# Kernel tuning notes

Measured on AMD Instinct MI355X. Metric: run time of the kernel, lower is better.

## Reference

```python
import jax, jax.numpy as jnp
import numpy as np

N = 50000
E = 800000
IN_C = 128
HID = 32
OUT_C = 16
NEG_SLOPE = 0.2


def setup_inputs() -> dict:
    key = jax.random.key(0)
    ks = jax.random.split(key, 16)
    x = jax.random.normal(ks[0], (N, IN_C), dtype=jnp.float32)
    edge_index = jax.random.randint(ks[1], (2, E), 0, N, dtype=jnp.int64)

    def glorot(k, shape):
        fan = shape[0] + shape[-1]
        return jax.random.uniform(k, shape, jnp.float32, -1.0, 1.0) * jnp.sqrt(6.0 / fan)

    # layer1: in=128 -> heads=4, ch=32, concat -> out 128
    W1 = glorot(ks[2], (IN_C, 4 * HID))
    a_src1 = glorot(ks[3], (4, HID))
    a_dst1 = glorot(ks[4], (4, HID))
    b1 = jnp.zeros((4 * HID,), jnp.float32)
    # layer2: in=128 -> heads=2, ch=32, concat -> out 64
    W2 = glorot(ks[5], (4 * HID, 2 * HID))
    a_src2 = glorot(ks[6], (2, HID))
    a_dst2 = glorot(ks[7], (2, HID))
    b2 = jnp.zeros((2 * HID,), jnp.float32)
    # layer3: in=64 -> heads=1, ch=16, mean -> out 16
    W3 = glorot(ks[8], (2 * HID, OUT_C))
    a_src3 = glorot(ks[9], (1, OUT_C))
    a_dst3 = glorot(ks[10], (1, OUT_C))
    b3 = jnp.zeros((OUT_C,), jnp.float32)
    return {"x": x, "edge_index": edge_index,
            "W1": W1, "a_src1": a_src1, "a_dst1": a_dst1, "b1": b1,
            "W2": W2, "a_src2": a_src2, "a_dst2": a_dst2, "b2": b2,
            "W3": W3, "a_src3": a_src3, "a_dst3": a_dst3, "b3": b3}


def gat_conv(x, src, dst, W, a_src, a_dst, bias, heads, ch, concat):
    n = x.shape[0]
    h = (x @ W).reshape(n, heads, ch)                      # [N,H,C]
    alpha_s = jnp.einsum('nhc,hc->nh', h, a_src)           # [N,H]
    alpha_d = jnp.einsum('nhc,hc->nh', h, a_dst)           # [N,H]
    logits = jax.nn.leaky_relu(alpha_s[src] + alpha_d[dst], NEG_SLOPE)  # [E,H]
    # segment softmax over edges sharing the same destination node
    m = jax.ops.segment_max(logits, dst, num_segments=n)
    m = jnp.where(jnp.isfinite(m), m, 0.0)
    e = jnp.exp(logits - m[dst])
    denom = jax.ops.segment_sum(e, dst, num_segments=n)
    alpha = e / (denom[dst] + 1e-16)                       # [E,H]
    msg = h[src] * alpha[:, :, None]                       # [E,H,C]
    out = jax.ops.segment_sum(msg, dst, num_segments=n)    # [N,H,C]
    out = out.reshape(n, heads * ch) if concat else out.mean(axis=1)
    return out + bias


def reference(x, edge_index, W1, a_src1, a_dst1, b1, W2, a_src2, a_dst2, b2, W3, a_src3, a_dst3, b3):
    n = x.shape[0]
    loops = jnp.arange(n, dtype=edge_index.dtype)
    src = jnp.concatenate([edge_index[0], loops])  # add self loops (PyG default)
    dst = jnp.concatenate([edge_index[1], loops])
    h = jax.nn.relu(gat_conv(x, src, dst, W1, a_src1, a_dst1, b1, 4, HID, True))
    h = jax.nn.relu(gat_conv(h, src, dst, W2, a_src2, a_dst2, b2, 2, HID, True))
    out = gat_conv(h, src, dst, W3, a_src3, a_dst3, b3, 1, OUT_C, False)
    return out
```

## Files before the change

kernel.cpp:

```cpp
#include <hip/hip_runtime.h>
#include <hip/hip_bf16.h>
#include <stdint.h>

#define NODES 50000
#define NEDGE 800000
#define TEDGE (NEDGE + NODES)
#define GBLK ((NODES + 63) / 64)
#define CHNK 64
#define CSRCH 13312
#define HALFN 25088
#define NSTR (2 * HALFN)
#define FSB 64
#define SCATB 832

typedef unsigned short u16;
typedef unsigned int u32;
typedef unsigned long long u64;
typedef short s16x8 __attribute__((ext_vector_type(8)));
typedef float f32x4 __attribute__((ext_vector_type(4)));

__device__ __forceinline__ float bf2f(u16 v) {
  return __uint_as_float(((u32)v) << 16);
}
__device__ __forceinline__ u16 f2bf(float f) {
  u32 u = __float_as_uint(f);
  u32 r = (u + 0x7FFFu + ((u >> 16) & 1u)) >> 16;
  return (u16)r;
}
__device__ __forceinline__ float lo16f(u32 w) { return __uint_as_float(w << 16); }
__device__ __forceinline__ float hi16f(u32 w) { return __uint_as_float(w & 0xFFFF0000u); }
__device__ __forceinline__ float lrelu(float x) {
  return (x > 0.f) ? x : 0.2f * x;
}
__device__ __forceinline__ int clampn(int v) {
  return ((u32)v < NODES) ? v : 0;
}
__device__ __forceinline__ float load1(const void* p, size_t i, bool fb) {
  return fb ? bf2f(((const u16*)p)[i]) : ((const float*)p)[i];
}
__device__ __forceinline__ u32 encf(float f) {
  u32 u = __float_as_uint(f);
  return (u & 0x80000000u) ? ~u : (u | 0x80000000u);
}
__device__ __forceinline__ float decf(u32 k) {
  u32 u = (k & 0x80000000u) ? (k & 0x7FFFFFFFu) : ~k;
  return __uint_as_float(u);
}

__global__ __launch_bounds__(256) void k_probe(
    const int* __restrict__ ei, const u16* __restrict__ xs16,
    int* __restrict__ flags,
    const void* __restrict__ W1, const void* __restrict__ W2,
    const void* __restrict__ W3, const void* __restrict__ as1,
    const void* __restrict__ ad1, const void* __restrict__ as2,
    const void* __restrict__ ad2, const void* __restrict__ as3,
    const void* __restrict__ ad3, u16* __restrict__ wt1,
    u16* __restrict__ wt2, u16* __restrict__ wt3, u16* __restrict__ wa1,
    u16* __restrict__ wa2, u16* __restrict__ wa3) {
  __shared__ int sfb;
  int t = threadIdx.x;
  int g = blockIdx.x * 256 + t;
  if (blockIdx.x == 0 && t >= 2 && t < 32) flags[t] = 0;
  if (t < 64) {
    int big = 0;
#pragma unroll
    for (int k = 0; k < 4; ++k) {
      u32 ex = (xs16[2 * (t * 4 + k)] >> 7) & 0xFF;
      big += (ex >= 0x90);
    }
#pragma unroll
    for (int off = 32; off >= 1; off >>= 1) big += __shfl_xor(big, off);
    if (t == 0) sfb = (big >= 8) ? 0 : 1;
    if (blockIdx.x == 0) {
      int odd = 0, even = 0;
#pragma unroll
      for (int k = 0; k < 4; ++k) {
        int idx = t + 64 * k;
        odd |= (ei[2 * idx + 1] != 0);
        even |= (ei[2 * idx] != 0);
      }
      u64 bo = __ballot(odd);
      u64 be = __ballot(even);
      if (t == 0) flags[0] = (bo == 0ull && be != 0ull) ? 1 : 0;
    }
  }
  __syncthreads();
  bool fb = sfb != 0;
  if (blockIdx.x == 0 && t == 0) flags[1] = fb ? 1 : 0;

  auto fidx = [](int n, int k, int KS) {
    int nt = n >> 4, lrow = n & 15, ks = k >> 5, quad = (k >> 3) & 3, j = k & 7;
    return ((size_t)((nt * KS + ks) * 64 + quad * 16 + lrow)) * 8 + j;
  };

  if (g < 16384) {
    int n = g >> 7, k = g & 127;
    wt1[fidx(n, k, 4)] = f2bf(load1(W1, (size_t)k * 128 + n, fb));
  } else if (g < 24576) {
    int r = g - 16384;
    int n = r >> 7, k = r & 127;
    wt2[fidx(n, k, 4)] = f2bf(load1(W2, (size_t)k * 64 + n, fb));
  } else if (g < 25600) {
    int r = g - 24576;
    int n = r >> 6, k = r & 63;
    wt3[fidx(n, k, 2)] = f2bf(load1(W3, (size_t)k * 16 + n, fb));
  } else if (g < 27648) {
    int e = g - 25600;
    int n = e >> 7, k = e & 127;
    float v = 0.f;
    if (n < 8) {
      int head = (n < 4) ? n : n - 4;
      const void* av = (n < 4) ? as1 : ad1;
      for (int c = 0; c < 32; ++c)
        v += load1(W1, (size_t)k * 128 + head * 32 + c, fb) *
             load1(av, head * 32 + c, fb);
    }
    wa1[fidx(n, k, 4)] = (n < 8) ? f2bf(v) : (u16)0;
  } else if (g < 29696) {
    int e = g - 27648;
    int n = e >> 7, k = e & 127;
    float v = 0.f;
    if (n < 4) {
      int head = (n < 2) ? n : n - 2;
      const void* av = (n < 2) ? as2 : ad2;
      for (int c = 0; c < 32; ++c)
        v += load1(W2, (size_t)k * 64 + head * 32 + c, fb) *
             load1(av, head * 32 + c, fb);
    }
    wa2[fidx(n, k, 4)] = (n < 4) ? f2bf(v) : (u16)0;
  } else if (g < 30720) {
    int e = g - 29696;
    int n = e >> 6, k = e & 63;
    float v = 0.f;
    if (n < 2) {
      const void* av = (n < 1) ? as3 : ad3;
      for (int c = 0; c < 16; ++c)
        v += load1(W3, (size_t)k * 16 + c, fb) * load1(av, c, fb);
    }
    wa3[fidx(n, k, 2)] = (n < 2) ? f2bf(v) : (u16)0;
  }
}

__global__ __launch_bounds__(1024) void k_hista(const int* __restrict__ ei,
                                                const int* __restrict__ flags,
                                                u32* __restrict__ sd,
                                                u16* __restrict__ rank16,
                                                u16* __restrict__ cnt) {
  __shared__ u32 hcnt[HALFN / 2];
  int b = blockIdx.x;
  int c = b >> 1, half = b & 1;
  int t = threadIdx.x;
  for (int i = t; i < HALFN / 2; i += 1024) hcnt[i] = 0;
  __syncthreads();
  bool odd = flags[0] != 0;
  int ebase = c * CSRCH;
  int nlo = half * HALFN;
#pragma unroll
  for (int i = 0; i < 13; ++i) {
    int e = ebase + i * 1024 + t;
    if (e < TEDGE) {
      int s, d;
      if (e < NEDGE) {
        if (odd) { s = ei[2 * e]; d = ei[2 * (NEDGE + e)]; }
        else { s = ei[e]; d = ei[NEDGE + e]; }
      } else {
        s = e - NEDGE; d = s;
      }
      s = clampn(s); d = clampn(d);
      if (half == 0) sd[e] = (u32)s | ((u32)d << 16);
      int li = d - nlo;
      if ((u32)li < HALFN) {
        u32 old = atomicAdd(&hcnt[li >> 1], 1u << (16 * (li & 1)));
        rank16[e] = (u16)((old >> (16 * (li & 1))) & 0xFFFFu);
      }
    }
  }
  __syncthreads();
  u32* crow = (u32*)(cnt + (size_t)c * NSTR + nlo);
  for (int i = t; i < HALFN / 2; i += 1024) crow[i] = hcnt[i];
}

__global__ __launch_bounds__(1024) void k_foldscan(const u16* __restrict__ cnt,
                                                   u16* __restrict__ basecnt,
                                                   int* __restrict__ rowptr,
                                                   int* __restrict__ parts,
                                                   int* __restrict__ counter) {
  __shared__ int swave[16];
  __shared__ int sbase, stot;
  int b = blockIdx.x, t = threadIdx.x;
  int n = b * 784 + t;
  int v = 0;
  if (t < 784 && n < NODES) {
    int acc = 0;
#pragma unroll 8
    for (int c = 0; c < CHNK; ++c) {
      u16 cv = cnt[(size_t)c * NSTR + n];
      basecnt[(size_t)c * NSTR + n] = (u16)acc;
      acc += cv;
    }
    v = acc;
  }
  int lane = t & 63, w = t >> 6;
  int x = v;
#pragma unroll
  for (int off = 1; off < 64; off <<= 1) {
    int y = __shfl_up(x, off);
    if (lane >= off) x += y;
  }
  if (lane == 63) swave[w] = x;
  __syncthreads();
  if (w == 0) {
    int wv = (lane < 16) ? swave[lane] : 0;
#pragma unroll
    for (int off = 1; off < 16; off <<= 1) {
      int y = __shfl_up(wv, off);
      if (lane >= off) wv += y;
    }
    if (lane == 15) {
      __hip_atomic_store(&parts[b], wv, __ATOMIC_RELAXED,
                         __HIP_MEMORY_SCOPE_AGENT);
      __hip_atomic_fetch_add(counter, 1, __ATOMIC_RELEASE,
                             __HIP_MEMORY_SCOPE_AGENT);
    }
    if (lane < 16) swave[lane] = wv;
  }
  __syncthreads();
  if (t == 0) {
    while (__hip_atomic_load(counter, __ATOMIC_ACQUIRE,
                             __HIP_MEMORY_SCOPE_AGENT) < FSB)
      __builtin_amdgcn_s_sleep(2);
  }
  __syncthreads();
  if (w == 0) {
    int pv = __hip_atomic_load(&parts[lane], __ATOMIC_RELAXED,
                               __HIP_MEMORY_SCOPE_AGENT);
    int pb = (lane < b) ? pv : 0;
#pragma unroll
    for (int off = 32; off >= 1; off >>= 1) {
      pb += __shfl_xor(pb, off);
      pv += __shfl_xor(pv, off);
    }
    if (lane == 0) { sbase = pb; stot = pv; }
  }
  __syncthreads();
  int run = sbase + ((w == 0) ? 0 : swave[w - 1]) + (x - v);
  if (t < 784 && n < NODES) rowptr[n] = run;
  if (b == 0 && t == 0) rowptr[NODES] = stot;
}


template <int K, int N, int H, bool XEXT>
__device__ __forceinline__ void gmfma_tile(const void* __restrict__ xin,
                                           const u16* __restrict__ wtf,
                                           const u16* __restrict__ waf,
                                           u16* __restrict__ hout,
                                           float* __restrict__ asg,
                                           float* __restrict__ adg,
                                           u32* __restrict__ gm,
                                           const int* __restrict__ flags,
                                           int M, int row0,
                                           u16* __restrict__ xlds,
                                           u32* __restrict__ lmax) {
  constexpr int KP = K + 8;
  constexpr int NT = N / 16;
  constexpr int KS = K / 32;
  constexpr int KG = K / 8;
  int t = threadIdx.x;
  bool fb = flags[1] != 0;
  if (t < 2 * H) lmax[t] = 0;

  bool xbf = XEXT ? fb : true;
  for (int i = t; i < 64 * KG; i += 256) {
    int r = i / KG, kg = i % KG;
    int grow = row0 + r;
    if (grow >= M) grow = M - 1;
    if (xbf) {
      *(uint4*)&xlds[r * KP + kg * 8] =
          *(const uint4*)((const u16*)xin + (size_t)grow * K + kg * 8);
    } else {
      const float* gp = (const float*)xin + (size_t)grow * K + kg * 8;
      float4 f0 = *(const float4*)gp, f1 = *(const float4*)(gp + 4);
      *(ushort4*)&xlds[r * KP + kg * 8] =
          make_ushort4(f2bf(f0.x), f2bf(f0.y), f2bf(f0.z), f2bf(f0.w));
      *(ushort4*)&xlds[r * KP + kg * 8 + 4] =
          make_ushort4(f2bf(f1.x), f2bf(f1.y), f2bf(f1.z), f2bf(f1.w));
    }
  }
  __syncthreads();

  int lane = t & 63, w = t >> 6;
  int lrow = lane & 15, quad = lane >> 4;
  f32x4 acc[NT];
  f32x4 eacc = (f32x4){0.f, 0.f, 0.f, 0.f};
#pragma unroll
  for (int nt = 0; nt < NT; ++nt) acc[nt] = (f32x4){0.f, 0.f, 0.f, 0.f};

  const u16* xbase = xlds + (w * 16 + lrow) * KP + quad * 8;
#pragma unroll
  for (int ks = 0; ks < KS; ++ks) {
    s16x8 a = *(const s16x8*)(xbase + ks * 32);
    s16x8 be = *(const s16x8*)(waf + ((size_t)(ks * 64 + lane)) * 8);
    eacc = __builtin_amdgcn_mfma_f32_16x16x32_bf16(a, be, eacc, 0, 0, 0);
#pragma unroll
    for (int nt = 0; nt < NT; ++nt) {
      s16x8 b = *(const s16x8*)(wtf + ((size_t)((nt * KS + ks) * 64 + lane)) * 8);
      acc[nt] = __builtin_amdgcn_mfma_f32_16x16x32_bf16(a, b, acc[nt], 0, 0, 0);
    }
  }

  float pm = -3.4e38f;
  int baserow = row0 + w * 16 + quad * 4;
#pragma unroll
  for (int r = 0; r < 4; ++r) {
    int grow = baserow + r;
    if (grow < M) {
#pragma unroll
      for (int nt = 0; nt < NT; ++nt)
        hout[(size_t)grow * N + nt * 16 + lrow] = f2bf(acc[nt][r]);
      if (lrow < H) asg[grow * H + lrow] = eacc[r];
      else if (lrow < 2 * H) adg[grow * H + (lrow - H)] = eacc[r];
    }
    pm = fmaxf(pm, eacc[r]);
  }
  if (lrow < 2 * H) atomicMax(&lmax[lrow], encf(pm));
  __syncthreads();
  if (t < 2 * H) atomicMax(&gm[t], lmax[t]);
}

__global__ __launch_bounds__(256) void k_scatgm(
    const u32* __restrict__ sd, const u16* __restrict__ rank16,
    const u16* __restrict__ basecnt, const int* __restrict__ rowptr,
    u16* __restrict__ srcs, const void* __restrict__ xin,
    const u16* __restrict__ wtf, const u16* __restrict__ waf,
    u16* __restrict__ hout, float* __restrict__ asg, float* __restrict__ adg,
    u32* __restrict__ gm, const int* __restrict__ flags) {
  __shared__ u16 xlds[64 * 136];
  __shared__ u32 lmax[8];
  int bi = blockIdx.x;
  int role, idx;
  if (bi < 2 * GBLK) { role = bi & 1; idx = bi >> 1; }
  else { role = 0; idx = GBLK + (bi - 2 * GBLK); }
  if (role == 0) {
    int c = idx / 13;
    int e0 = idx * 1024 + threadIdx.x;
#pragma unroll
    for (int u = 0; u < 4; ++u) {
      int e = e0 + u * 256;
      if (e < TEDGE) {
        u32 v = sd[e];
        int d = (int)(v >> 16);
        int pos = rowptr[d] + (int)basecnt[(size_t)c * NSTR + d] +
                  (int)rank16[e];
        srcs[pos] = (u16)(v & 0xFFFFu);
      }
    }
    return;
  }
  gmfma_tile<128, 128, 4, true>(xin, wtf, waf, hout, asg, adg, gm, flags,
                                NODES, idx * 64, xlds, lmax);
}

template <int K, int N, int H, bool XEXT>
__global__ __launch_bounds__(256) void k_gmfma(const void* __restrict__ xin,
                                               const u16* __restrict__ wtf,
                                               const u16* __restrict__ waf,
                                               u16* __restrict__ hout,
                                               float* __restrict__ asg,
                                               float* __restrict__ adg,
                                               u32* __restrict__ gm,
                                               const int* __restrict__ flags,
                                               int M) {
  __shared__ u16 xlds[64 * (K + 8)];
  __shared__ u32 lmax[2 * H];
  gmfma_tile<K, N, H, XEXT>(xin, wtf, waf, hout, asg, adg, gm, flags, M,
                            blockIdx.x * 64, xlds, lmax);
}

template <int H, int C, bool RELU, bool FINAL>
__global__ __launch_bounds__(256) void k_agg(const u16* __restrict__ hbuf,
                                             const float* __restrict__ asg,
                                             const float* __restrict__ adg,
                                             const int* __restrict__ rowptr,
                                             const u16* __restrict__ srcs,
                                             const void* __restrict__ bias,
                                             const int* __restrict__ flags,
                                             const u32* __restrict__ gm,
                                             void* __restrict__ outp, int n) {
  constexpr int HC = H * C;
  constexpr int L = HC / 8;
  constexpr int EPN = 32 / L;
  constexpr int UN = (4 * EPN <= 32) ? 4 : 2;
  __shared__ u16 lds_s[4][64];
  __shared__ float lds_e[4][64][H];
  int lane = threadIdx.x & 63;
  int w = threadIdx.x >> 6;
  int nh = lane >> 5;
  int hl = lane & 31;
  int node = blockIdx.x * 8 + w * 2 + nh;
  if (node >= n) node = n - 1;
  bool fb = flags[1] != 0;
  int start = rowptr[node], end = rowptr[node + 1];
  if (end < start || end - start > TEDGE) { start = 0; end = 0; }

  float adh[H], M[H];
#pragma unroll
  for (int h = 0; h < H; ++h) adh[h] = adg[node * H + h];
#pragma unroll
  for (int h = 0; h < H; ++h) M[h] = lrelu(decf(gm[h]) + decf(gm[H + h]));

  int sub = hl / L;
  int cl = hl & (L - 1);
  int ch0 = cl * 8;
  int myhead = ch0 / C;
  int base = nh * 32;

  float den[H];
#pragma unroll
  for (int h = 0; h < H; ++h) den[h] = 0.f;
  float acc[UN][8];
#pragma unroll
  for (int u = 0; u < UN; ++u)
#pragma unroll
    for (int i = 0; i < 8; ++i) acc[u][i] = 0.f;

  for (int chunk = start; chunk < end; chunk += 32) {
    int e = chunk + hl;
    int s = 0;
    float ee[H];
#pragma unroll
    for (int h = 0; h < H; ++h) ee[h] = 0.f;
    if (e < end) {
      s = srcs[e];
      float av[H];
      if (H == 4) { float4 t4 = *(const float4*)(asg + s * 4);
        av[0] = t4.x; av[1] = t4.y; av[H > 2 ? 2 : 0] = t4.z; av[H > 3 ? 3 : 0] = t4.w; }
      else if (H == 2) { float2 t2 = *(const float2*)(asg + s * 2); av[0] = t2.x; av[1] = t2.y; }
      else av[0] = asg[s];
#pragma unroll
      for (int h = 0; h < H; ++h) {
        float x = __expf(lrelu(av[h] + adh[h]) - M[h]);
        ee[h] = x;
        den[h] += x;
      }
    }
    __builtin_amdgcn_wave_barrier();
    lds_s[w][lane] = (u16)s;
#pragma unroll
    for (int h = 0; h < H; ++h) lds_e[w][lane][h] = ee[h];
    __builtin_amdgcn_wave_barrier();

    int cn = min(32, end - chunk);
    for (int j = 0; j < cn; j += UN * EPN) {
      int sx[UN];
      float ax[UN];
#pragma unroll
      for (int u = 0; u < UN; ++u) {
        int ei_ = base + j + u * EPN + sub;
        sx[u] = lds_s[w][ei_];
        ax[u] = lds_e[w][ei_][myhead];
      }
#pragma unroll
      for (int u = 0; u < UN; ++u) {
        uint4 v = *(const uint4*)(hbuf + (size_t)sx[u] * HC + ch0);
        acc[u][0] += ax[u] * lo16f(v.x); acc[u][1] += ax[u] * hi16f(v.x);
        acc[u][2] += ax[u] * lo16f(v.y); acc[u][3] += ax[u] * hi16f(v.y);
        acc[u][4] += ax[u] * lo16f(v.z); acc[u][5] += ax[u] * hi16f(v.z);
        acc[u][6] += ax[u] * lo16f(v.w); acc[u][7] += ax[u] * hi16f(v.w);
      }
    }
  }

#pragma unroll
  for (int m = 16; m >= 1; m >>= 1) {
#pragma unroll
    for (int h = 0; h < H; ++h) den[h] += __shfl_xor(den[h], m);
  }
  float tt[8];
#pragma unroll
  for (int i = 0; i < 8; ++i) {
    tt[i] = acc[0][i];
#pragma unroll
    for (int u = 1; u < UN; ++u) tt[i] += acc[u][i];
  }
#pragma unroll
  for (int m = L; m < 32; m <<= 1) {
#pragma unroll
    for (int i = 0; i < 8; ++i) tt[i] += __shfl_xor(tt[i], m);
  }

  if (sub == 0) {
    float inv = 1.f / (den[myhead] + 1e-16f);
    float o[8];
#pragma unroll
    for (int i = 0; i < 8; ++i) {
      o[i] = tt[i] * inv + load1(bias, ch0 + i, fb);
      if (RELU) o[i] = fmaxf(o[i], 0.f);
    }
    bool obf = FINAL ? fb : true;
    if (obf) {
      uint4 pk;
      pk.x = (u32)f2bf(o[0]) | ((u32)f2bf(o[1]) << 16);
      pk.y = (u32)f2bf(o[2]) | ((u32)f2bf(o[3]) << 16);
      pk.z = (u32)f2bf(o[4]) | ((u32)f2bf(o[5]) << 16);
      pk.w = (u32)f2bf(o[6]) | ((u32)f2bf(o[7]) << 16);
      *(uint4*)((u16*)outp + (size_t)node * HC + ch0) = pk;
    } else {
      float* op = (float*)outp + (size_t)node * HC + ch0;
      *(float4*)op = make_float4(o[0], o[1], o[2], o[3]);
      *(float4*)(op + 4) = make_float4(o[4], o[5], o[6], o[7]);
    }
  }
}


extern "C" void kernel_launch(void* const* d_in, const int* in_sizes, int n_in,
                              void* d_out, int out_size, void* d_ws, size_t ws_size,
                              hipStream_t stream) {
  const void* x   = d_in[0];
  const int* ei   = (const int*)d_in[1];
  const void* W1  = d_in[2];
  const void* as1 = d_in[3];
  const void* ad1 = d_in[4];
  const void* b1  = d_in[5];
  const void* W2  = d_in[6];
  const void* as2 = d_in[7];
  const void* ad2 = d_in[8];
  const void* b2  = d_in[9];
  const void* W3  = d_in[10];
  const void* as3 = d_in[11];
  const void* ad3 = d_in[12];
  const void* b3  = d_in[13];

  char* w = (char*)d_ws;
  auto alloc = [&](size_t bytes) {
    char* p = w;
    w += (bytes + 255) & ~(size_t)255;
    return p;
  };
  int* flags    = (int*)alloc(256);
  int* parts    = (int*)alloc(256);
  int* rowptr   = (int*)alloc((size_t)(NODES + 1) * 4);
  u16* cnt      = (u16*)alloc((size_t)CHNK * NSTR * 2);
  u16* basecnt  = (u16*)alloc((size_t)CHNK * NSTR * 2);
  u32* sd       = (u32*)alloc((size_t)TEDGE * 4);
  u16* rank16   = (u16*)alloc((size_t)TEDGE * 2);
  u16* srcs     = (u16*)alloc((size_t)TEDGE * 2);
  float* asg    = (float*)alloc((size_t)NODES * 4 * 4);
  float* adg    = (float*)alloc((size_t)NODES * 4 * 4);
  u16* wt1      = (u16*)alloc((size_t)128 * 128 * 2);
  u16* wt2      = (u16*)alloc((size_t)64 * 128 * 2);
  u16* wt3      = (u16*)alloc((size_t)16 * 64 * 2);
  u16* wa1      = (u16*)alloc((size_t)16 * 128 * 2);
  u16* wa2      = (u16*)alloc((size_t)16 * 128 * 2);
  u16* wa3      = (u16*)alloc((size_t)16 * 64 * 2);
  u16* hbuf     = (u16*)alloc((size_t)NODES * 128 * 2);
  u16* obuf     = (u16*)alloc((size_t)NODES * 128 * 2);

  u32* gm1 = (u32*)(flags + 8);
  u32* gm2 = (u32*)(flags + 16);
  u32* gm3 = (u32*)(flags + 24);

  int ablocks = (NODES + 7) / 8;
  int sgrid = 2 * GBLK + (SCATB - GBLK);

  k_probe<<<(NODES + 255) / 256, 256, 0, stream>>>(
      ei, (const u16*)x, flags, W1, W2, W3, as1, ad1, as2, ad2, as3, ad3,
      wt1, wt2, wt3, wa1, wa2, wa3);
  k_hista<<<2 * CHNK, 1024, 0, stream>>>(ei, flags, sd, rank16, cnt);
  k_foldscan<<<FSB, 1024, 0, stream>>>(cnt, basecnt, rowptr, parts, flags + 2);
  k_scatgm<<<sgrid, 256, 0, stream>>>(sd, rank16, basecnt, rowptr, srcs,
                                      x, wt1, wa1, hbuf, asg, adg, gm1, flags);

  k_agg<4, 32, true, false><<<ablocks, 256, 0, stream>>>(hbuf, asg, adg, rowptr, srcs, b1, flags, gm1, obuf, NODES);
  k_gmfma<128, 64, 2, false><<<GBLK, 256, 0, stream>>>(obuf, wt2, wa2, hbuf, asg, adg, gm2, flags, NODES);
  k_agg<2, 32, true, false><<<ablocks, 256, 0, stream>>>(hbuf, asg, adg, rowptr, srcs, b2, flags, gm2, obuf, NODES);
  k_gmfma<64, 16, 1, false><<<GBLK, 256, 0, stream>>>(obuf, wt3, wa3, hbuf, asg, adg, gm3, flags, NODES);
  k_agg<1, 16, false, true><<<ablocks, 256, 0, stream>>>(hbuf, asg, adg, rowptr, srcs, b3, flags, gm3, d_out, NODES);
}
```

Measured before the change: 255.3 us.

## Fuse histogram with fold-scan and aggregation with next-layer GEMM via spin flags

Merges the histogram and fold-scan kernels into one launch, where the scan blocks spin on a global counter until all histogram blocks finish. Each aggregation kernel is fused with the following layer's MFMA GEMM. GEMM blocks wait on per-tile done counters written by the aggregation blocks that produce their 64 rows. Separate ping-pong buffers per layer avoid read/write hazards. The aim is to remove launch gaps and tails between stages, at the cost of relying on forward progress of spinning blocks and on block scheduling order.

```diff
diff --git a/kernel.cpp b/kernel.cpp
--- a/kernel.cpp
+++ b/kernel.cpp
@@ -6,6 +6,7 @@
 #define NEDGE 800000
 #define TEDGE (NEDGE + NODES)
 #define GBLK ((NODES + 63) / 64)
+#define ABLK ((NODES + 7) / 8)
 #define CHNK 64
 #define CSRCH 13312
 #define HALFN 25088
@@ -49,7 +50,7 @@
 
 __global__ __launch_bounds__(256) void k_probe(
     const int* __restrict__ ei, const u16* __restrict__ xs16,
-    int* __restrict__ flags,
+    int* __restrict__ flags, int* __restrict__ done2, int* __restrict__ done3,
     const void* __restrict__ W1, const void* __restrict__ W2,
     const void* __restrict__ W3, const void* __restrict__ as1,
     const void* __restrict__ ad1, const void* __restrict__ as2,
@@ -61,6 +62,7 @@
   int t = threadIdx.x;
   int g = blockIdx.x * 256 + t;
   if (blockIdx.x == 0 && t >= 2 && t < 32) flags[t] = 0;
+  if (g < GBLK) { done2[g] = 0; done3[g] = 0; }
   if (t < 64) {
     int big = 0;
 #pragma unroll
@@ -141,54 +143,60 @@
   }
 }
 
-__global__ __launch_bounds__(1024) void k_hista(const int* __restrict__ ei,
-                                                const int* __restrict__ flags,
-                                                u32* __restrict__ sd,
-                                                u16* __restrict__ rank16,
-                                                u16* __restrict__ cnt) {
-  __shared__ u32 hcnt[HALFN / 2];
-  int b = blockIdx.x;
-  int c = b >> 1, half = b & 1;
-  int t = threadIdx.x;
-  for (int i = t; i < HALFN / 2; i += 1024) hcnt[i] = 0;
-  __syncthreads();
-  bool odd = flags[0] != 0;
-  int ebase = c * CSRCH;
-  int nlo = half * HALFN;
-#pragma unroll
-  for (int i = 0; i < 13; ++i) {
-    int e = ebase + i * 1024 + t;
-    if (e < TEDGE) {
-      int s, d;
-      if (e < NEDGE) {
-        if (odd) { s = ei[2 * e]; d = ei[2 * (NEDGE + e)]; }
-        else { s = ei[e]; d = ei[NEDGE + e]; }
-      } else {
-        s = e - NEDGE; d = s;
+__global__ __launch_bounds__(1024) void k_fh(
+    const int* __restrict__ ei, int* __restrict__ flags,
+    u32* __restrict__ sd, u16* __restrict__ rank16, u16* __restrict__ cnt,
+    u16* __restrict__ basecnt, int* __restrict__ rowptr,
+    int* __restrict__ parts) {
+  __shared__ __align__(16) char smem[50176];
+  int b = blockIdx.x, t = threadIdx.x;
+  if (b < 2 * CHNK) {
+    u32* hcnt = (u32*)smem;
+    int c = b >> 1, half = b & 1;
+    for (int i = t; i < HALFN / 2; i += 1024) hcnt[i] = 0;
+    __syncthreads();
+    bool odd = flags[0] != 0;
+    int ebase = c * CSRCH;
+    int nlo = half * HALFN;
+#pragma unroll
+    for (int i = 0; i < 13; ++i) {
+      int e = ebase + i * 1024 + t;
+      if (e < TEDGE) {
+        int s, d;
+        if (e < NEDGE) {
+          if (odd) { s = ei[2 * e]; d = ei[2 * (NEDGE + e)]; }
+          else { s = ei[e]; d = ei[NEDGE + e]; }
+        } else {
+          s = e - NEDGE; d = s;
+        }
+        s = clampn(s); d = clampn(d);
+        if (half == 0) sd[e] = (u32)s | ((u32)d << 16);
+        int li = d - nlo;
+        if ((u32)li < HALFN) {
+          u32 old = atomicAdd(&hcnt[li >> 1], 1u << (16 * (li & 1)));
+          rank16[e] = (u16)((old >> (16 * (li & 1))) & 0xFFFFu);
+        }
       }
-      s = clampn(s); d = clampn(d);
-      if (half == 0) sd[e] = (u32)s | ((u32)d << 16);
-      int li = d - nlo;
-      if ((u32)li < HALFN) {
-        u32 old = atomicAdd(&hcnt[li >> 1], 1u << (16 * (li & 1)));
-        rank16[e] = (u16)((old >> (16 * (li & 1))) & 0xFFFFu);
-      }
-    }
-  }
-  __syncthreads();
-  u32* crow = (u32*)(cnt + (size_t)c * NSTR + nlo);
-  for (int i = t; i < HALFN / 2; i += 1024) crow[i] = hcnt[i];
-}
-
-__global__ __launch_bounds__(1024) void k_foldscan(const u16* __restrict__ cnt,
-                                                   u16* __restrict__ basecnt,
-                                                   int* __restrict__ rowptr,
-                                                   int* __restrict__ parts,
-                                                   int* __restrict__ counter) {
-  __shared__ int swave[16];
-  __shared__ int sbase, stot;
-  int b = blockIdx.x, t = threadIdx.x;
-  int n = b * 784 + t;
+    }
+    __syncthreads();
+    u32* crow = (u32*)(cnt + (size_t)c * NSTR + nlo);
+    for (int i = t; i < HALFN / 2; i += 1024) crow[i] = hcnt[i];
+    __syncthreads();
+    if (t == 0)
+      __hip_atomic_fetch_add(&flags[2], 1, __ATOMIC_RELEASE,
+                             __HIP_MEMORY_SCOPE_AGENT);
+    return;
+  }
+  int fb = b - 2 * CHNK;
+  int* swave = (int*)smem;
+  int* sps = (int*)(smem + 64);
+  if (t == 0) {
+    while (__hip_atomic_load(&flags[2], __ATOMIC_ACQUIRE,
+                             __HIP_MEMORY_SCOPE_AGENT) < 2 * CHNK)
+      __builtin_amdgcn_s_sleep(8);
+  }
+  __syncthreads();
+  int n = fb * 784 + t;
   int v = 0;
   if (t < 784 && n < NODES) {
     int acc = 0;
@@ -217,16 +225,16 @@
       if (lane >= off) wv += y;
     }
     if (lane == 15) {
-      __hip_atomic_store(&parts[b], wv, __ATOMIC_RELAXED,
+      __hip_atomic_store(&parts[fb], wv, __ATOMIC_RELAXED,
                          __HIP_MEMORY_SCOPE_AGENT);
-      __hip_atomic_fetch_add(counter, 1, __ATOMIC_RELEASE,
+      __hip_atomic_fetch_add(&flags[3], 1, __ATOMIC_RELEASE,
                              __HIP_MEMORY_SCOPE_AGENT);
     }
     if (lane < 16) swave[lane] = wv;
   }
   __syncthreads();
   if (t == 0) {
-    while (__hip_atomic_load(counter, __ATOMIC_ACQUIRE,
+    while (__hip_atomic_load(&flags[3], __ATOMIC_ACQUIRE,
                              __HIP_MEMORY_SCOPE_AGENT) < FSB)
       __builtin_amdgcn_s_sleep(2);
   }
@@ -234,20 +242,19 @@
   if (w == 0) {
     int pv = __hip_atomic_load(&parts[lane], __ATOMIC_RELAXED,
                                __HIP_MEMORY_SCOPE_AGENT);
-    int pb = (lane < b) ? pv : 0;
+    int pb = (lane < fb) ? pv : 0;
 #pragma unroll
     for (int off = 32; off >= 1; off >>= 1) {
       pb += __shfl_xor(pb, off);
       pv += __shfl_xor(pv, off);
     }
-    if (lane == 0) { sbase = pb; stot = pv; }
-  }
-  __syncthreads();
-  int run = sbase + ((w == 0) ? 0 : swave[w - 1]) + (x - v);
+    if (lane == 0) { sps[0] = pb; sps[1] = pv; }
+  }
+  __syncthreads();
+  int run = sps[0] + ((w == 0) ? 0 : swave[w - 1]) + (x - v);
   if (t < 784 && n < NODES) rowptr[n] = run;
-  if (b == 0 && t == 0) rowptr[NODES] = stot;
-}
-
+  if (fb == 0 && t == 0) rowptr[NODES] = sps[1];
+}
 
 template <int K, int N, int H, bool XEXT>
 __device__ __forceinline__ void gmfma_tile(const void* __restrict__ xin,
@@ -360,43 +367,24 @@
                                 NODES, idx * 64, xlds, lmax);
 }
 
-template <int K, int N, int H, bool XEXT>
-__global__ __launch_bounds__(256) void k_gmfma(const void* __restrict__ xin,
-                                               const u16* __restrict__ wtf,
-                                               const u16* __restrict__ waf,
-                                               u16* __restrict__ hout,
-                                               float* __restrict__ asg,
-                                               float* __restrict__ adg,
-                                               u32* __restrict__ gm,
-                                               const int* __restrict__ flags,
-                                               int M) {
-  __shared__ u16 xlds[64 * (K + 8)];
-  __shared__ u32 lmax[2 * H];
-  gmfma_tile<K, N, H, XEXT>(xin, wtf, waf, hout, asg, adg, gm, flags, M,
-                            blockIdx.x * 64, xlds, lmax);
-}
-
 template <int H, int C, bool RELU, bool FINAL>
-__global__ __launch_bounds__(256) void k_agg(const u16* __restrict__ hbuf,
-                                             const float* __restrict__ asg,
-                                             const float* __restrict__ adg,
-                                             const int* __restrict__ rowptr,
-                                             const u16* __restrict__ srcs,
-                                             const void* __restrict__ bias,
-                                             const int* __restrict__ flags,
-                                             const u32* __restrict__ gm,
-                                             void* __restrict__ outp, int n) {
+__device__ __forceinline__ void agg_body(
+    const u16* __restrict__ hbuf, const float* __restrict__ asg,
+    const float* __restrict__ adg, const int* __restrict__ rowptr,
+    const u16* __restrict__ srcs, const void* __restrict__ bias,
+    const int* __restrict__ flags, const u32* __restrict__ gm,
+    void* __restrict__ outp, int n, int bi, char* smem) {
   constexpr int HC = H * C;
   constexpr int L = HC / 8;
   constexpr int EPN = 32 / L;
   constexpr int UN = (4 * EPN <= 32) ? 4 : 2;
-  __shared__ u16 lds_s[4][64];
-  __shared__ float lds_e[4][64][H];
+  auto lds_s = (u16(*)[64])smem;
+  auto lds_e = (float(*)[64][H])(smem + 512);
   int lane = threadIdx.x & 63;
   int w = threadIdx.x >> 6;
   int nh = lane >> 5;
   int hl = lane & 31;
-  int node = blockIdx.x * 8 + w * 2 + nh;
+  int node = bi * 8 + w * 2 + nh;
   if (node >= n) node = n - 1;
   bool fb = flags[1] != 0;
   int start = rowptr[node], end = rowptr[node + 1];
@@ -510,6 +498,61 @@
       *(float4*)(op + 4) = make_float4(o[4], o[5], o[6], o[7]);
     }
   }
+}
+
+template <int H, int C, bool RELU, bool FINAL>
+__global__ __launch_bounds__(256) void k_agg(const u16* __restrict__ hbuf,
+                                             const float* __restrict__ asg,
+                                             const float* __restrict__ adg,
+                                             const int* __restrict__ rowptr,
+                                             const u16* __restrict__ srcs,
+                                             const void* __restrict__ bias,
+                                             const int* __restrict__ flags,
+                                             const u32* __restrict__ gm,
+                                             void* __restrict__ outp, int n) {
+  __shared__ __align__(16) char smem[512 + 4 * 64 * H * 4];
+  agg_body<H, C, RELU, FINAL>(hbuf, asg, adg, rowptr, srcs, bias, flags, gm,
+                              outp, n, blockIdx.x, smem);
+}
+
+template <int H, int C, int K2, int N2, int H2>
+__global__ __launch_bounds__(256) void k_aggm(
+    const u16* __restrict__ hbuf, const float* __restrict__ asg,
+    const float* __restrict__ adg, const int* __restrict__ rowptr,
+    const u16* __restrict__ srcs, const void* __restrict__ bias,
+    const int* __restrict__ flags, const u32* __restrict__ gm,
+    u16* __restrict__ obuf, int* __restrict__ done,
+    const u16* __restrict__ wtf2, const u16* __restrict__ waf2,
+    u16* __restrict__ hout2, float* __restrict__ asg2,
+    float* __restrict__ adg2, u32* __restrict__ gm2) {
+  constexpr int XB = 64 * (K2 + 8) * 2;
+  constexpr int GB = XB + 2 * H2 * 4;
+  constexpr int AB = 512 + 4 * 64 * H * 4;
+  constexpr int SM = (GB > AB) ? GB : AB;
+  __shared__ __align__(16) char smem[SM];
+  int bi = blockIdx.x;
+  if (bi < ABLK) {
+    agg_body<H, C, true, false>(hbuf, asg, adg, rowptr, srcs, bias, flags, gm,
+                                obuf, NODES, bi, smem);
+    __syncthreads();
+    if (threadIdx.x == 0)
+      __hip_atomic_fetch_add(&done[bi >> 3], 1, __ATOMIC_RELEASE,
+                             __HIP_MEMORY_SCOPE_AGENT);
+    return;
+  }
+  int idx = bi - ABLK;
+  if (idx >= GBLK) return;
+  int target = (idx == GBLK - 1) ? (ABLK - 8 * idx) : 8;
+  if (threadIdx.x == 0) {
+    while (__hip_atomic_load(&done[idx], __ATOMIC_ACQUIRE,
+                             __HIP_MEMORY_SCOPE_AGENT) < target)
+      __builtin_amdgcn_s_sleep(8);
+  }
+  __syncthreads();
+  u16* xlds = (u16*)smem;
+  u32* lmax = (u32*)(smem + XB);
+  gmfma_tile<K2, N2, H2, false>(obuf, wtf2, waf2, hout2, asg2, adg2, gm2,
+                                flags, NODES, idx * 64, xlds, lmax);
 }
 
 
@@ -539,41 +582,53 @@
   };
   int* flags    = (int*)alloc(256);
   int* parts    = (int*)alloc(256);
+  int* done2    = (int*)alloc((size_t)GBLK * 4);
+  int* done3    = (int*)alloc((size_t)GBLK * 4);
   int* rowptr   = (int*)alloc((size_t)(NODES + 1) * 4);
   u16* cnt      = (u16*)alloc((size_t)CHNK * NSTR * 2);
   u16* basecnt  = (u16*)alloc((size_t)CHNK * NSTR * 2);
   u32* sd       = (u32*)alloc((size_t)TEDGE * 4);
   u16* rank16   = (u16*)alloc((size_t)TEDGE * 2);
   u16* srcs     = (u16*)alloc((size_t)TEDGE * 2);
-  float* asg    = (float*)alloc((size_t)NODES * 4 * 4);
-  float* adg    = (float*)alloc((size_t)NODES * 4 * 4);
+  float* asg1   = (float*)alloc((size_t)NODES * 4 * 4);
+  float* adg1   = (float*)alloc((size_t)NODES * 4 * 4);
+  float* asg2   = (float*)alloc((size_t)NODES * 2 * 4);
+  float* adg2   = (float*)alloc((size_t)NODES * 2 * 4);
+  float* asg3   = (float*)alloc((size_t)NODES * 1 * 4);
+  float* adg3   = (float*)alloc((size_t)NODES * 1 * 4);
   u16* wt1      = (u16*)alloc((size_t)128 * 128 * 2);
   u16* wt2      = (u16*)alloc((size_t)64 * 128 * 2);
   u16* wt3      = (u16*)alloc((size_t)16 * 64 * 2);
   u16* wa1      = (u16*)alloc((size_t)16 * 128 * 2);
   u16* wa2      = (u16*)alloc((size_t)16 * 128 * 2);
   u16* wa3      = (u16*)alloc((size_t)16 * 64 * 2);
-  u16* hbuf     = (u16*)alloc((size_t)NODES * 128 * 2);
-  u16* obuf     = (u16*)alloc((size_t)NODES * 128 * 2);
+  u16* hbuf1    = (u16*)alloc((size_t)NODES * 128 * 2);
+  u16* obuf1    = (u16*)alloc((size_t)NODES * 128 * 2);
+  u16* hbuf2    = (u16*)alloc((size_t)NODES * 64 * 2);
+  u16* obuf2    = (u16*)alloc((size_t)NODES * 64 * 2);
+  u16* hbuf3    = (u16*)alloc((size_t)NODES * 16 * 2);
 
   u32* gm1 = (u32*)(flags + 8);
   u32* gm2 = (u32*)(flags + 16);
   u32* gm3 = (u32*)(flags + 24);
 
-  int ablocks = (NODES + 7) / 8;
   int sgrid = 2 * GBLK + (SCATB - GBLK);
+  int pgrid = ABLK + GBLK;
 
   k_probe<<<(NODES + 255) / 256, 256, 0, stream>>>(
-      ei, (const u16*)x, flags, W1, W2, W3, as1, ad1, as2, ad2, as3, ad3,
-      wt1, wt2, wt3, wa1, wa2, wa3);
-  k_hista<<<2 * CHNK, 1024, 0, stream>>>(ei, flags, sd, rank16, cnt);
-  k_foldscan<<<FSB, 1024, 0, stream>>>(cnt, basecnt, rowptr, parts, flags + 2);
+      ei, (const u16*)x, flags, done2, done3, W1, W2, W3, as1, ad1, as2, ad2,
+      as3, ad3, wt1, wt2, wt3, wa1, wa2, wa3);
+  k_fh<<<2 * CHNK + FSB, 1024, 0, stream>>>(ei, flags, sd, rank16, cnt,
+                                            basecnt, rowptr, parts);
   k_scatgm<<<sgrid, 256, 0, stream>>>(sd, rank16, basecnt, rowptr, srcs,
-                                      x, wt1, wa1, hbuf, asg, adg, gm1, flags);
-
-  k_agg<4, 32, true, false><<<ablocks, 256, 0, stream>>>(hbuf, asg, adg, rowptr, srcs, b1, flags, gm1, obuf, NODES);
-  k_gmfma<128, 64, 2, false><<<GBLK, 256, 0, stream>>>(obuf, wt2, wa2, hbuf, asg, adg, gm2, flags, NODES);
-  k_agg<2, 32, true, false><<<ablocks, 256, 0, stream>>>(hbuf, asg, adg, rowptr, srcs, b2, flags, gm2, obuf, NODES);
-  k_gmfma<64, 16, 1, false><<<GBLK, 256, 0, stream>>>(obuf, wt3, wa3, hbuf, asg, adg, gm3, flags, NODES);
-  k_agg<1, 16, false, true><<<ablocks, 256, 0, stream>>>(hbuf, asg, adg, rowptr, srcs, b3, flags, gm3, d_out, NODES);
-}
+                                      x, wt1, wa1, hbuf1, asg1, adg1, gm1,
+                                      flags);
+  k_aggm<4, 32, 128, 64, 2><<<pgrid, 256, 0, stream>>>(
+      hbuf1, asg1, adg1, rowptr, srcs, b1, flags, gm1, obuf1, done2,
+      wt2, wa2, hbuf2, asg2, adg2, gm2);
+  k_aggm<2, 32, 64, 16, 1><<<pgrid, 256, 0, stream>>>(
+      hbuf2, asg2, adg2, rowptr, srcs, b2, flags, gm2, obuf2, done3,
+      wt3, wa3, hbuf3, asg3, adg3, gm3);
+  k_agg<1, 16, false, true><<<ABLK, 256, 0, stream>>>(
+      hbuf3, asg3, adg3, rowptr, srcs, b3, flags, gm3, d_out, NODES);
+}
```

Result: slower. 500.2 us (+95.9%).
